# Kernel optimization log

Measured on AMD Instinct MI355X. Metric: run time of the kernel, lower is better.

Reference implementation:

```python
import jax, jax.numpy as jnp
import numpy as np
from jax import lax

RADIUS = [1, 3, 5, 9, 13, 21]
RATE = 1
K = 4            # shift radius -> (2K+1)^2 = 81 shifts
EPS = 1e-8       # torch.cosine_similarity eps


def setup_inputs() -> dict:
    key = jax.random.key(0)
    k1, k2, k3, k4 = jax.random.split(key, 4)
    b, cin, cout, h, w = 2, 128, 128, 96, 128
    x = jax.random.normal(k1, (b, cout, h, w), dtype=jnp.float32)
    y = jax.random.normal(k2, (b, cin, h, w), dtype=jnp.float32)
    # 6 dilated conv branches, all Conv2d(cin, cout, 3) -> stacked (6, O, I, 3, 3)
    weights = jax.random.normal(k3, (6, cout, cin, 3, 3), dtype=jnp.float32) * 0.05
    biases = jax.random.normal(k4, (6, cout), dtype=jnp.float32) * 0.05
    return {"x": x, "y": y, "weights": weights, "biases": biases}


def _forward(x, y, weights, biases):
    b, c, h, w = y.shape
    k = K
    # reflect-pad y by k, then 'same' dilated convs (zero padding = dilation)
    y_pad = jnp.pad(y, ((0, 0), (0, 0), (k, k), (k, k)), mode="reflect")

    # precompute grouped query features and their norms once
    xg = x.reshape(b, 4, -1, h, w)                      # (b,4,c/4,h,w)
    xn = jnp.sqrt(jnp.sum(xg * xg, axis=2))             # (b,4,h,w)

    # per-branch conv outputs over the padded extent, grouped, with cached norms
    branches = []
    for idx, r in enumerate(RADIUS):
        d = r * RATE
        yo = lax.conv_general_dilated(
            y_pad, weights[idx], window_strides=(1, 1),
            padding=[(d, d), (d, d)], rhs_dilation=(d, d),
            dimension_numbers=("NCHW", "OIHW", "NCHW"),
        ) + biases[idx][None, :, None, None]            # (b,cout,h+2k,w+2k)
        yg = yo.reshape(b, 4, -1, h + 2 * k, w + 2 * k)
        yn = jnp.sqrt(jnp.sum(yg * yg, axis=2))          # (b,4,h+2k,w+2k)
        branches.append((yg, yn))

    result = []
    for i in range(-k, k + 1):
        for j in range(-k, k + 1):
            sx, sy = k + i, k + j
            corrs = []
            for yg, yn in branches:
                ygs = yg[:, :, :, sx:sx + h, sy:sy + w]
                yns = yn[:, :, sx:sx + h, sy:sy + w]
                dot = jnp.einsum("bgchw,bgchw->bghw", xg, ygs)
                corrs.append(dot / jnp.maximum(xn * yns, EPS))
            result.append(jnp.concatenate(corrs, axis=1))  # (b,24,h,w)
    return jnp.stack(result, axis=2)                       # (b,24,81,h,w)


def reference(x, y, weights, biases):
    return _forward(x, y, weights, biases)
```

## Files before the change

kernel.cpp:

```cpp
#include <hip/hip_runtime.h>
#include <math.h>

#define B 2
#define CH 128
#define H 96
#define W 128
#define HP 104
#define WP 136
#define KPAD 4
#define NSHIFT 81
#define NBR 6
#define HW (H*W)
#define HWP (HP*WP)
#define NTILE 111

typedef _Float16 h2 __attribute__((ext_vector_type(2)));
typedef _Float16 half8 __attribute__((ext_vector_type(8)));
typedef float floatx4 __attribute__((ext_vector_type(4)));

__device__ __constant__ int d_radius[NBR] = {1, 3, 5, 9, 13, 21};

__device__ __forceinline__ void async16(const _Float16* g, _Float16* l) {
    __builtin_amdgcn_global_load_lds(
        (const __attribute__((address_space(1))) unsigned int*)g,
        (__attribute__((address_space(3))) unsigned int*)l, 16, 0, 0);
}

__global__ __launch_bounds__(256) void prep_y(const float* __restrict__ y,
                                              _Float16* __restrict__ yt16) {
    __shared__ h2 tile[64 * 129];
    const int tid = threadIdx.x;
    const int b = blockIdx.y;
    const int pix0 = blockIdx.x * 128;
    const int half = tid >> 7;
    const int pl = tid & 127;

    const float* yb = y + (size_t)b * CH * HW + pix0 + pl;
    #pragma unroll
    for (int k = 0; k < 32; ++k) {
        int c = half * 64 + 2 * k;
        float v0 = yb[(size_t)c * HW];
        float v1 = yb[(size_t)(c + 1) * HW];
        h2 v; v[0] = (_Float16)v0; v[1] = (_Float16)v1;
        tile[(half * 32 + k) * 129 + pl] = v;
    }
    __syncthreads();

    _Float16* ob = yt16 + ((size_t)b * HW + pix0) * CH;
    #pragma unroll
    for (int it = 0; it < 8; ++it) {
        int pix = it * 16 + (tid >> 4);
        int c2b = (tid & 15) * 4;
        h2 t0 = tile[(c2b + 0) * 129 + pix];
        h2 t1 = tile[(c2b + 1) * 129 + pix];
        h2 t2 = tile[(c2b + 2) * 129 + pix];
        h2 t3 = tile[(c2b + 3) * 129 + pix];
        half8 o;
        o[0] = t0[0]; o[1] = t0[1]; o[2] = t1[0]; o[3] = t1[1];
        o[4] = t2[0]; o[5] = t2[1]; o[6] = t3[0]; o[7] = t3[1];
        *(half8*)(ob + (size_t)pix * CH + (tid & 15) * 8) = o;
    }
}

__global__ __launch_bounds__(256) void convert_w_kernel(const float* __restrict__ w,
                                                        _Float16* __restrict__ w16t,
                                                        _Float16* __restrict__ zbuf) {
    int gid = blockIdx.x * 256 + threadIdx.x;
    if (gid < 256) zbuf[gid] = (_Float16)0.0f;
    if (gid >= NBR * 9 * CH * CH) return;
    int ci = gid & 127;
    int co = (gid >> 7) & 127;
    int rest = gid >> 14;
    int tap = rest % 9;
    int br = rest / 9;
    w16t[gid] = (_Float16)w[(((size_t)(br * CH + co)) * CH + ci) * 9 + tap];
}

__global__ __launch_bounds__(256) void prep_x(const float* __restrict__ x,
                                              h2* __restrict__ xh,
                                              float* __restrict__ xn) {
    const int b = blockIdx.y;
    const int pix = blockIdx.x * 256 + threadIdx.x;
    const float* xb = x + (size_t)b * CH * HW + pix;
    #pragma unroll
    for (int g = 0; g < 4; ++g) {
        float s = 0.f;
        #pragma unroll
        for (int p = 0; p < 16; ++p) {
            int c = g * 32 + 2 * p;
            float v0 = xb[(size_t)c * HW];
            float v1 = xb[(size_t)(c + 1) * HW];
            h2 v; v[0] = (_Float16)v0; v[1] = (_Float16)v1;
            xh[((size_t)((b * 4 + g) * 16 + p)) * HW + pix] = v;
            s += v0 * v0 + v1 * v1;
        }
        xn[(size_t)(b * 4 + g) * HW + pix] = sqrtf(s);
    }
}

__global__ __launch_bounds__(256) void conv_mfma(const _Float16* __restrict__ yt16,
                                                 const _Float16* __restrict__ w16t,
                                                 const _Float16* __restrict__ zbuf,
                                                 const float* __restrict__ biases,
                                                 h2* __restrict__ ygh,
                                                 float* __restrict__ yn_all) {
    const int tid = threadIdx.x;
    const int lane = tid & 63;
    const int wv = tid >> 6;
    const int tile = blockIdx.x;
    const int br = blockIdx.y;
    const int b = blockIdx.z;
    const int d = d_radius[br];
    const int px0 = tile * 128;

    __shared__ __align__(16) _Float16 Al[128 * 32];
    __shared__ __align__(16) _Float16 Bl[128 * 32];

    const int l16 = tid & 3;
    int ph[2], pw[2];
    bool pval[2];
    #pragma unroll
    for (int s = 0; s < 2; ++s) {
        int pixl = s * 64 + (tid >> 2);
        int pix = px0 + pixl;
        pval[s] = pix < HWP;
        int phh = pix / WP;
        ph[s] = phh; pw[s] = pix - phh * WP;
    }

    const _Float16* ytb = yt16 + (size_t)b * HW * CH;
    const _Float16* wbr = w16t + (size_t)br * 9 * CH * CH;

    floatx4 acc[4][4];
    #pragma unroll
    for (int i = 0; i < 4; i++)
        #pragma unroll
        for (int j = 0; j < 4; j++) {
            floatx4 z = {0.f, 0.f, 0.f, 0.f};
            acc[i][j] = z;
        }

    const int mrow = (wv & 1) * 64 + (lane & 15);
    const int ncol = (wv >> 1) * 64 + (lane & 15);
    const int kq = (lane >> 4) * 8;

    for (int tap = 0; tap < 9; ++tap) {
        const int dkh = (tap / 3 - 1) * d;
        const int dkw = (tap % 3 - 1) * d;
        const _Float16* brow[2];
        #pragma unroll
        for (int s = 0; s < 2; ++s) {
            int gr = ph[s] + dkh, gc = pw[s] + dkw;
            bool v = pval[s] && ((unsigned)gr < (unsigned)HP) && ((unsigned)gc < (unsigned)WP);
            const _Float16* p;
            if (v) {
                int yr = gr - KPAD; yr = yr < 0 ? -yr : (yr >= H ? 2 * (H - 1) - yr : yr);
                int yc = gc - KPAD; yc = yc < 0 ? -yc : (yc >= W ? 2 * (W - 1) - yc : yc);
                p = ytb + ((size_t)(yr * W + yc)) * CH + l16 * 8;
            } else {
                p = zbuf + l16 * 8;
            }
            brow[s] = p;
        }
        const _Float16* wa = wbr + tap * CH * CH + (tid >> 2) * CH + l16 * 8;

        for (int ck = 0; ck < 4; ++ck) {
            const int ci0 = ck * 32;
            async16(wa + ci0,            Al + wv * 512);
            async16(wa + 64 * CH + ci0,  Al + 2048 + wv * 512);
            async16(brow[0] + ci0,       Bl + wv * 512);
            async16(brow[1] + ci0,       Bl + 2048 + wv * 512);
            __syncthreads();

            half8 af[4], bf[4];
            #pragma unroll
            for (int i = 0; i < 4; i++) af[i] = *(const half8*)&Al[(mrow + i * 16) * 32 + kq];
            #pragma unroll
            for (int j = 0; j < 4; j++) bf[j] = *(const half8*)&Bl[(ncol + j * 16) * 32 + kq];
            #pragma unroll
            for (int i = 0; i < 4; i++)
                #pragma unroll
                for (int j = 0; j < 4; j++)
                    acc[i][j] = __builtin_amdgcn_mfma_f32_16x16x32_f16(af[i], bf[j], acc[i][j], 0, 0, 0);
            __syncthreads();
        }
    }

    float yna[2][4];
    #pragma unroll
    for (int gs = 0; gs < 2; ++gs)
        #pragma unroll
        for (int j = 0; j < 4; ++j) yna[gs][j] = 0.f;

    #pragma unroll
    for (int i = 0; i < 4; i++) {
        int m0 = (wv & 1) * 64 + i * 16 + (lane >> 4) * 4;
        int g0 = (m0 >> 5);
        int pp = (m0 & 31) >> 1;
        float b0 = biases[br * CH + m0];
        float b1 = biases[br * CH + m0 + 1];
        float b2 = biases[br * CH + m0 + 2];
        float b3 = biases[br * CH + m0 + 3];
        h2* outp = ygh + (((size_t)(br * B + b) * 4 + g0) * 16 + pp) * HWP;
        #pragma unroll
        for (int j = 0; j < 4; j++) {
            int pix = px0 + (wv >> 1) * 64 + j * 16 + (lane & 15);
            if (pix < HWP) {
                float f0 = acc[i][j][0] + b0;
                float f1 = acc[i][j][1] + b1;
                float f2 = acc[i][j][2] + b2;
                float f3 = acc[i][j][3] + b3;
                yna[i >> 1][j] += f0 * f0 + f1 * f1 + f2 * f2 + f3 * f3;
                h2 v0, v1;
                v0[0] = (_Float16)f0;
                v0[1] = (_Float16)f1;
                v1[0] = (_Float16)f2;
                v1[1] = (_Float16)f3;
                outp[pix] = v0;
                outp[(size_t)HWP + pix] = v1;
            }
        }
    }

    #pragma unroll
    for (int gs = 0; gs < 2; ++gs) {
        #pragma unroll
        for (int j = 0; j < 4; ++j) {
            float s = yna[gs][j];
            s += __shfl_xor(s, 16);
            s += __shfl_xor(s, 32);
            if ((lane >> 4) == 0) {
                int pix = px0 + (wv >> 1) * 64 + j * 16 + lane;
                if (pix < HWP) {
                    int g = (wv & 1) * 2 + gs;
                    yn_all[((size_t)((br * B + b) * 4 + g)) * HWP + pix] = sqrtf(s);
                }
            }
        }
    }
}

#define CPAIR 4
__global__ __launch_bounds__(256) void corr2_kernel(const h2* __restrict__ xh,
                                                    const h2* __restrict__ ygh,
                                                    const float* __restrict__ xn,
                                                    const float* __restrict__ yn_all,
                                                    float* __restrict__ out) {
    const int tid = threadIdx.x;
    const int row = tid >> 5;
    const int col4 = (tid & 31) * 4;
    const int H0 = blockIdx.x * 8;
    const int bg = blockIdx.y;
    const int g = bg & 3, b = bg >> 2;
    const int brl = blockIdx.z;
    const int hh = H0 + row;

    __shared__ __align__(16) _Float16 yt[CPAIR * 340 * 8];

    const h2* ygb = ygh + ((size_t)((brl * B + b) * 4 + g) * 16) * HWP;
    const h2* xb  = xh  + ((size_t)(b * 4 + g) * 16) * HW;
    const float* ynb = yn_all + (size_t)((brl * B + b) * 4 + g) * HWP;

    float xnv[4];
    *(floatx4*)xnv = *(const floatx4*)(xn + (size_t)(b * 4 + g) * HW + hh * W + col4);

    for (int chunk = 0; chunk < 3; ++chunk) {
        const int row0 = H0 + chunk * 3;
        float acc[108];
        #pragma unroll
        for (int s = 0; s < 108; ++s) acc[s] = 0.f;

        for (int p0 = 0; p0 < 16; p0 += CPAIR) {
            __syncthreads();
            for (int i = tid; i < CPAIR * 340; i += 256) {
                int pr = i / 340, off = i - pr * 340;
                const _Float16* src =
                    (const _Float16*)(ygb + (size_t)(p0 + pr) * HWP + row0 * WP) + off * 8;
                async16(src, yt + i * 8);
            }
            __syncthreads();
            #pragma unroll
            for (int cp = 0; cp < CPAIR; ++cp) {
                h2 x2[4];
                *(half8*)x2 = *(const half8*)(xb + (size_t)(p0 + cp) * HW + hh * W + col4);
                #pragma unroll
                for (int sx = 0; sx < 3; ++sx) {
                    h2 yv[12];
                    const _Float16* yr = yt + (cp * 1360 + (row + sx) * 136 + col4) * 2;
                    ((half8*)yv)[0] = *(const half8*)(yr);
                    ((half8*)yv)[1] = *(const half8*)(yr + 8);
                    ((half8*)yv)[2] = *(const half8*)(yr + 16);
                    #pragma unroll
                    for (int sy = 0; sy < 9; ++sy)
                        #pragma unroll
                        for (int j = 0; j < 4; ++j)
                            acc[(sx * 9 + sy) * 4 + j] = __builtin_amdgcn_fdot2(
                                x2[j], yv[sy + j], acc[(sx * 9 + sy) * 4 + j], false);
                }
            }
        }

        #pragma unroll
        for (int sxl = 0; sxl < 3; ++sxl) {
            int sx = chunk * 3 + sxl;
            float ynv[12];
            const float* yp = ynb + (size_t)(hh + sx) * WP + col4;
            *(floatx4*)&ynv[0] = *(const floatx4*)(yp);
            *(floatx4*)&ynv[4] = *(const floatx4*)(yp + 4);
            *(floatx4*)&ynv[8] = *(const floatx4*)(yp + 8);
            float* ob = out + ((size_t)(b * 24 + brl * 4 + g) * NSHIFT + sx * 9) * HW
                        + hh * W + col4;
            #pragma unroll
            for (int sy = 0; sy < 9; ++sy) {
                float o[4];
                #pragma unroll
                for (int j = 0; j < 4; ++j) {
                    float den = xnv[j] * ynv[j + sy];
                    den = den > 1e-8f ? den : 1e-8f;
                    o[j] = acc[(sxl * 9 + sy) * 4 + j] / den;
                }
                *(floatx4*)(ob + (size_t)sy * HW) = *(floatx4*)o;
            }
        }
    }
}

extern "C" void kernel_launch(void* const* d_in, const int* in_sizes, int n_in,
                              void* d_out, int out_size, void* d_ws, size_t ws_size,
                              hipStream_t stream) {
    const float* x       = (const float*)d_in[0];
    const float* y       = (const float*)d_in[1];
    const float* weights = (const float*)d_in[2];
    const float* biases  = (const float*)d_in[3];
    float* out = (float*)d_out;

    const size_t ygh_b = (size_t)NBR * B * 4 * 16 * HWP * 4;
    const size_t yn_b  = (size_t)NBR * B * 4 * HWP * 4;
    const size_t xn_b  = (size_t)B * 4 * HW * 4;
    const size_t yt_b  = (size_t)B * HW * CH * 2;
    const size_t wt_b  = (size_t)NBR * 9 * CH * CH * 2;
    const size_t xh_b  = (size_t)B * 4 * 16 * HW * 4;

    char* p = (char*)d_ws;
    h2* ygh       = (h2*)p;       p += ygh_b;
    float* yn_all = (float*)p;    p += yn_b;
    float* xn     = (float*)p;    p += xn_b;
    _Float16* yt16 = (_Float16*)p; p += yt_b;
    _Float16* w16t = (_Float16*)p; p += wt_b;
    h2* xh        = (h2*)p;       p += xh_b;
    _Float16* zbuf = (_Float16*)p;

    prep_y<<<dim3(HW / 128, B), 256, 0, stream>>>(y, yt16);
    convert_w_kernel<<<(NBR * 9 * CH * CH + 255) / 256, 256, 0, stream>>>(weights, w16t, zbuf);
    prep_x<<<dim3(HW / 256, B), 256, 0, stream>>>(x, xh, xn);

    conv_mfma<<<dim3(NTILE, NBR, B), 256, 0, stream>>>(yt16, w16t, zbuf, biases, ygh, yn_all);

    corr2_kernel<<<dim3(12, 8, NBR), 256, 0, stream>>>(xh, ygh, xn, yn_all, out);
}
```

Baseline: 367.8 us.

## Double-buffer LDS loads in conv and correlation kernels, split chunks across blocks

The conv kernel now double-buffers its A/B tiles in LDS and prefetches the next K-chunk, including the next tap's rows, while MFMAs run on the current buffer. This drops one barrier per chunk. The correlation kernel also double-buffers its y tile staging. It moves the 3-chunk shift loop into the grid, giving three times as many blocks for occupancy. The cost is twice the LDS per block and redundant x loads across chunk blocks. The async global-to-LDS loads into the next buffer rely on the single barrier at the end of each iteration for correctness.

```diff
diff --git a/kernel.cpp b/kernel.cpp
--- a/kernel.cpp
+++ b/kernel.cpp
@@ -113,8 +113,8 @@
     const int d = d_radius[br];
     const int px0 = tile * 128;
 
-    __shared__ __align__(16) _Float16 Al[128 * 32];
-    __shared__ __align__(16) _Float16 Bl[128 * 32];
+    __shared__ __align__(16) _Float16 Al[2][128 * 32];
+    __shared__ __align__(16) _Float16 Bl[2][128 * 32];
 
     const int l16 = tid & 3;
     int ph[2], pw[2];
@@ -144,39 +144,59 @@
     const int ncol = (wv >> 1) * 64 + (lane & 15);
     const int kq = (lane >> 4) * 8;
 
-    for (int tap = 0; tap < 9; ++tap) {
+    auto comp_brow = [&](int tap, const _Float16*& o0, const _Float16*& o1) {
         const int dkh = (tap / 3 - 1) * d;
         const int dkw = (tap % 3 - 1) * d;
-        const _Float16* brow[2];
+        const _Float16* bw[2];
         #pragma unroll
         for (int s = 0; s < 2; ++s) {
             int gr = ph[s] + dkh, gc = pw[s] + dkw;
             bool v = pval[s] && ((unsigned)gr < (unsigned)HP) && ((unsigned)gc < (unsigned)WP);
-            const _Float16* p;
             if (v) {
                 int yr = gr - KPAD; yr = yr < 0 ? -yr : (yr >= H ? 2 * (H - 1) - yr : yr);
                 int yc = gc - KPAD; yc = yc < 0 ? -yc : (yc >= W ? 2 * (W - 1) - yc : yc);
-                p = ytb + ((size_t)(yr * W + yc)) * CH + l16 * 8;
+                bw[s] = ytb + ((size_t)(yr * W + yc)) * CH + l16 * 8;
             } else {
-                p = zbuf + l16 * 8;
-            }
-            brow[s] = p;
-        }
-        const _Float16* wa = wbr + tap * CH * CH + (tid >> 2) * CH + l16 * 8;
-
+                bw[s] = zbuf + l16 * 8;
+            }
+        }
+        o0 = bw[0]; o1 = bw[1];
+    };
+
+    const _Float16* bc0; const _Float16* bc1;
+    comp_brow(0, bc0, bc1);
+    const _Float16* wa = wbr + (tid >> 2) * CH + l16 * 8;
+
+    async16(wa,           Al[0] + wv * 512);
+    async16(wa + 64 * CH, Al[0] + 2048 + wv * 512);
+    async16(bc0,          Bl[0] + wv * 512);
+    async16(bc1,          Bl[0] + 2048 + wv * 512);
+    __syncthreads();
+
+    for (int tap = 0; tap < 9; ++tap) {
+        const _Float16* bn0 = bc0; const _Float16* bn1 = bc1;
+        #pragma unroll
         for (int ck = 0; ck < 4; ++ck) {
-            const int ci0 = ck * 32;
-            async16(wa + ci0,            Al + wv * 512);
-            async16(wa + 64 * CH + ci0,  Al + 2048 + wv * 512);
-            async16(brow[0] + ci0,       Bl + wv * 512);
-            async16(brow[1] + ci0,       Bl + 2048 + wv * 512);
-            __syncthreads();
-
+            const int cur = ck & 1;
+            const int nxt = cur ^ 1;
+            if (ck < 3) {
+                const int ci0 = (ck + 1) * 32;
+                async16(wa + ci0,           Al[nxt] + wv * 512);
+                async16(wa + 64 * CH + ci0, Al[nxt] + 2048 + wv * 512);
+                async16(bc0 + ci0,          Bl[nxt] + wv * 512);
+                async16(bc1 + ci0,          Bl[nxt] + 2048 + wv * 512);
+            } else if (tap < 8) {
+                comp_brow(tap + 1, bn0, bn1);
+                async16(wa + CH * CH,           Al[nxt] + wv * 512);
+                async16(wa + CH * CH + 64 * CH, Al[nxt] + 2048 + wv * 512);
+                async16(bn0,                    Bl[nxt] + wv * 512);
+                async16(bn1,                    Bl[nxt] + 2048 + wv * 512);
+            }
             half8 af[4], bf[4];
             #pragma unroll
-            for (int i = 0; i < 4; i++) af[i] = *(const half8*)&Al[(mrow + i * 16) * 32 + kq];
-            #pragma unroll
-            for (int j = 0; j < 4; j++) bf[j] = *(const half8*)&Bl[(ncol + j * 16) * 32 + kq];
+            for (int i = 0; i < 4; i++) af[i] = *(const half8*)&Al[cur][(mrow + i * 16) * 32 + kq];
+            #pragma unroll
+            for (int j = 0; j < 4; j++) bf[j] = *(const half8*)&Bl[cur][(ncol + j * 16) * 32 + kq];
             #pragma unroll
             for (int i = 0; i < 4; i++)
                 #pragma unroll
@@ -184,6 +204,8 @@
                     acc[i][j] = __builtin_amdgcn_mfma_f32_16x16x32_f16(af[i], bf[j], acc[i][j], 0, 0, 0);
             __syncthreads();
         }
+        bc0 = bn0; bc1 = bn1;
+        wa += CH * CH;
     }
 
     float yna[2][4];
@@ -252,10 +274,12 @@
     const int H0 = blockIdx.x * 8;
     const int bg = blockIdx.y;
     const int g = bg & 3, b = bg >> 2;
-    const int brl = blockIdx.z;
+    const int brl = blockIdx.z / 3;
+    const int chunk = blockIdx.z - brl * 3;
     const int hh = H0 + row;
-
-    __shared__ __align__(16) _Float16 yt[CPAIR * 340 * 8];
+    const int row0 = H0 + chunk * 3;
+
+    __shared__ __align__(16) _Float16 yt[2][CPAIR * 340 * 8];
 
     const h2* ygb = ygh + ((size_t)((brl * B + b) * 4 + g) * 16) * HWP;
     const h2* xb  = xh  + ((size_t)(b * 4 + g) * 16) * HW;
@@ -264,63 +288,73 @@
     float xnv[4];
     *(floatx4*)xnv = *(const floatx4*)(xn + (size_t)(b * 4 + g) * HW + hh * W + col4);
 
-    for (int chunk = 0; chunk < 3; ++chunk) {
-        const int row0 = H0 + chunk * 3;
-        float acc[108];
-        #pragma unroll
-        for (int s = 0; s < 108; ++s) acc[s] = 0.f;
-
-        for (int p0 = 0; p0 < 16; p0 += CPAIR) {
-            __syncthreads();
+    float acc[108];
+    #pragma unroll
+    for (int s = 0; s < 108; ++s) acc[s] = 0.f;
+
+    for (int i = tid; i < CPAIR * 340; i += 256) {
+        int pr = i / 340, off = i - pr * 340;
+        const _Float16* src =
+            (const _Float16*)(ygb + (size_t)pr * HWP + row0 * WP) + off * 8;
+        async16(src, yt[0] + i * 8);
+    }
+    __syncthreads();
+
+    #pragma unroll
+    for (int pi = 0; pi < 4; ++pi) {
+        const int cur = pi & 1;
+        if (pi < 3) {
+            const int p0n = (pi + 1) * CPAIR;
             for (int i = tid; i < CPAIR * 340; i += 256) {
                 int pr = i / 340, off = i - pr * 340;
                 const _Float16* src =
-                    (const _Float16*)(ygb + (size_t)(p0 + pr) * HWP + row0 * WP) + off * 8;
-                async16(src, yt + i * 8);
-            }
-            __syncthreads();
-            #pragma unroll
-            for (int cp = 0; cp < CPAIR; ++cp) {
-                h2 x2[4];
-                *(half8*)x2 = *(const half8*)(xb + (size_t)(p0 + cp) * HW + hh * W + col4);
+                    (const _Float16*)(ygb + (size_t)(p0n + pr) * HWP + row0 * WP) + off * 8;
+                async16(src, yt[cur ^ 1] + i * 8);
+            }
+        }
+        const int p0 = pi * CPAIR;
+        #pragma unroll
+        for (int cp = 0; cp < CPAIR; ++cp) {
+            h2 x2[4];
+            *(half8*)x2 = *(const half8*)(xb + (size_t)(p0 + cp) * HW + hh * W + col4);
+            #pragma unroll
+            for (int sx = 0; sx < 3; ++sx) {
+                h2 yv[12];
+                const _Float16* yr = yt[cur] + (cp * 1360 + (row + sx) * 136 + col4) * 2;
+                ((half8*)yv)[0] = *(const half8*)(yr);
+                ((half8*)yv)[1] = *(const half8*)(yr + 8);
+                ((half8*)yv)[2] = *(const half8*)(yr + 16);
                 #pragma unroll
-                for (int sx = 0; sx < 3; ++sx) {
-                    h2 yv[12];
-                    const _Float16* yr = yt + (cp * 1360 + (row + sx) * 136 + col4) * 2;
-                    ((half8*)yv)[0] = *(const half8*)(yr);
-                    ((half8*)yv)[1] = *(const half8*)(yr + 8);
-                    ((half8*)yv)[2] = *(const half8*)(yr + 16);
+                for (int sy = 0; sy < 9; ++sy)
                     #pragma unroll
-                    for (int sy = 0; sy < 9; ++sy)
-                        #pragma unroll
-                        for (int j = 0; j < 4; ++j)
-                            acc[(sx * 9 + sy) * 4 + j] = __builtin_amdgcn_fdot2(
-                                x2[j], yv[sy + j], acc[(sx * 9 + sy) * 4 + j], false);
-                }
-            }
-        }
-
-        #pragma unroll
-        for (int sxl = 0; sxl < 3; ++sxl) {
-            int sx = chunk * 3 + sxl;
-            float ynv[12];
-            const float* yp = ynb + (size_t)(hh + sx) * WP + col4;
-            *(floatx4*)&ynv[0] = *(const floatx4*)(yp);
-            *(floatx4*)&ynv[4] = *(const floatx4*)(yp + 4);
-            *(floatx4*)&ynv[8] = *(const floatx4*)(yp + 8);
-            float* ob = out + ((size_t)(b * 24 + brl * 4 + g) * NSHIFT + sx * 9) * HW
-                        + hh * W + col4;
-            #pragma unroll
-            for (int sy = 0; sy < 9; ++sy) {
-                float o[4];
-                #pragma unroll
-                for (int j = 0; j < 4; ++j) {
-                    float den = xnv[j] * ynv[j + sy];
-                    den = den > 1e-8f ? den : 1e-8f;
-                    o[j] = acc[(sxl * 9 + sy) * 4 + j] / den;
-                }
-                *(floatx4*)(ob + (size_t)sy * HW) = *(floatx4*)o;
-            }
+                    for (int j = 0; j < 4; ++j)
+                        acc[(sx * 9 + sy) * 4 + j] = __builtin_amdgcn_fdot2(
+                            x2[j], yv[sy + j], acc[(sx * 9 + sy) * 4 + j], false);
+            }
+        }
+        __syncthreads();
+    }
+
+    #pragma unroll
+    for (int sxl = 0; sxl < 3; ++sxl) {
+        int sx = chunk * 3 + sxl;
+        float ynv[12];
+        const float* yp = ynb + (size_t)(hh + sx) * WP + col4;
+        *(floatx4*)&ynv[0] = *(const floatx4*)(yp);
+        *(floatx4*)&ynv[4] = *(const floatx4*)(yp + 4);
+        *(floatx4*)&ynv[8] = *(const floatx4*)(yp + 8);
+        float* ob = out + ((size_t)(b * 24 + brl * 4 + g) * NSHIFT + sx * 9) * HW
+                    + hh * W + col4;
+        #pragma unroll
+        for (int sy = 0; sy < 9; ++sy) {
+            float o[4];
+            #pragma unroll
+            for (int j = 0; j < 4; ++j) {
+                float den = xnv[j] * ynv[j + sy];
+                den = den > 1e-8f ? den : 1e-8f;
+                o[j] = acc[(sxl * 9 + sy) * 4 + j] / den;
+            }
+            *(floatx4*)(ob + (size_t)sy * HW) = *(floatx4*)o;
         }
     }
 }
@@ -356,5 +390,5 @@
 
     conv_mfma<<<dim3(NTILE, NBR, B), 256, 0, stream>>>(yt16, w16t, zbuf, biases, ygh, yn_all);
 
-    corr2_kernel<<<dim3(12, 8, NBR), 256, 0, stream>>>(xh, ygh, xn, yn_all, out);
-}
+    corr2_kernel<<<dim3(12, 8, NBR * 3), 256, 0, stream>>>(xh, ygh, xn, yn_all, out);
+}
```

Result: faster. 354.8 us (-3.5%).
